# Optimization experiments

Measured on AMD Instinct MI355X. Metric: run time of the kernel, lower is better.

## Reference

```python
import jax, jax.numpy as jnp
import numpy as np

N = 100000   # nodes
E = 1600000  # edges (avg degree 16)
D = 128      # input feature dim
H = 64       # hidden dim (hard-coded in Sage.__init__)
C = 40       # output classes


def setup_inputs() -> dict:
    key = jax.random.key(0)
    ks = jax.random.split(key, 9)
    s_in = 1.0 / np.sqrt(D)
    s_h = 1.0 / np.sqrt(H)
    return {
        "x": jax.random.normal(ks[0], (N, D), jnp.float32),
        "edge_index": jax.random.randint(ks[1], (2, E), 0, N, dtype=jnp.int64),
        # SAGEConv params: lin_l acts on aggregated neighbors (carries bias),
        # lin_r acts on the root/self features (no bias), per PyG defaults.
        "W1_l": jax.random.uniform(ks[2], (D, H), jnp.float32, -s_in, s_in),
        "W1_r": jax.random.uniform(ks[3], (D, H), jnp.float32, -s_in, s_in),
        "b1": jax.random.uniform(ks[4], (H,), jnp.float32, -s_in, s_in),
        "W2_l": jax.random.uniform(ks[5], (H, C), jnp.float32, -s_h, s_h),
        "W2_r": jax.random.uniform(ks[6], (H, C), jnp.float32, -s_h, s_h),
        "b2": jax.random.uniform(ks[7], (C,), jnp.float32, -s_h, s_h),
    }


def _sage_conv(x, src, dst, W_l, W_r, b):
    # mean-aggregate neighbor features at destination nodes
    msg = x[src]                                             # [E, F] gather
    summed = jax.ops.segment_sum(msg, dst, num_segments=N)   # [N, F]
    deg = jax.ops.segment_sum(jnp.ones((src.shape[0],), x.dtype), dst,
                              num_segments=N)                # [N]
    agg = summed / jnp.maximum(deg, 1.0)[:, None]
    return agg @ W_l + x @ W_r + b


def reference(x, edge_index, W1_l, W1_r, b1, W2_l, W2_r, b2):
    src, dst = edge_index[0], edge_index[1]
    h = _sage_conv(x, src, dst, W1_l, W1_r, b1)
    h = jax.nn.relu(h)
    # F.dropout(training=False) in eval mode -> identity
    out = _sage_conv(h, src, dst, W2_l, W2_r, b2)
    return jax.nn.log_softmax(out, axis=1)
```

## Files before the change

kernel.cpp:

```cpp
#include <hip/hip_runtime.h>

__device__ __forceinline__ float bf2f(unsigned short u) {
  union { unsigned int i; float f; } c; c.i = ((unsigned int)u) << 16; return c.f;
}
__device__ __forceinline__ unsigned short f2bf(float f) {
  union { float f; unsigned int i; } c; c.f = f;
  unsigned int x = c.i;
  return (unsigned short)((x + 0x7fffu + ((x >> 16) & 1u)) >> 16);
}
__device__ __forceinline__ float lo16(unsigned int w) { return bf2f((unsigned short)(w & 0xffffu)); }
__device__ __forceinline__ float hi16(unsigned int w) { return bf2f((unsigned short)(w >> 16)); }

#define DD 128
#define HH 64
#define CC 40
#define NBUCK 512
#define NCHUNK 128
#define MAXNPB 256
#define NQ 4
#define NR 4
#define ECAP 6144

using bf16x8 = __attribute__((ext_vector_type(8))) short;
using f32x4  = __attribute__((ext_vector_type(4))) float;

__global__ __launch_bounds__(256) void detect_prepw(
    const unsigned int* e32, const unsigned int* x32, int* flags,
    const void* W1l, const void* W1r, const void* b1,
    const void* W2l, const void* W2r, const void* b2,
    unsigned short* Wb1, unsigned short* Wb2, float* b1f, float* b2f) {
  int tid = threadIdx.x;
  if (blockIdx.x == 0) {
    __shared__ unsigned int redOr[256];
    __shared__ int redCnt[256];
    unsigned int v = 0;
    for (int i = tid; i < 4096; i += 256) v |= e32[2 * i + 1];
    int cnt = 0;
    for (int i = tid; i < 4096; i += 256) {
      unsigned int w = x32[i];
      unsigned int expo = (w >> 7) & 0xffu;
      unsigned short lo = (unsigned short)(w & 0xffffu);
      if (lo == 0 || (expo >= 100u && expo <= 133u)) cnt++;
    }
    redOr[tid] = v; redCnt[tid] = cnt; __syncthreads();
    for (int s = 128; s > 0; s >>= 1) {
      if (tid < s) { redOr[tid] |= redOr[tid + s]; redCnt[tid] += redCnt[tid + s]; }
      __syncthreads();
    }
    if (tid == 0) {
      flags[0] = (redOr[0] == 0u) ? 1 : 0;
      flags[1] = (redCnt[0] < 2048) ? 1 : 0;
    }
    return;
  }
  __shared__ int red[256];
  const unsigned int* w32 = (const unsigned int*)W1l;
  int cnt = 0;
  for (int i = tid; i < 4096; i += 256) {
    unsigned int w = w32[i];
    unsigned int expo = (w >> 7) & 0xffu;
    unsigned short lo = (unsigned short)(w & 0xffffu);
    if (lo == 0 || (expo >= 100u && expo <= 133u)) cnt++;
  }
  red[tid] = cnt; __syncthreads();
  for (int s = 128; s > 0; s >>= 1) {
    if (tid < s) red[tid] += red[tid + s];
    __syncthreads();
  }
  int isf = (red[0] < 2048) ? 1 : 0;
  auto rd = [&](const void* p, int i) -> float {
    return isf ? ((const float*)p)[i] : bf2f(((const unsigned short*)p)[i]);
  };
  if (blockIdx.x == 1) {
    for (int idx = tid; idx < 128 * 128; idx += 256) {
      int n = idx >> 7, k = idx & 127;
      float v = (n < HH) ? rd(W1l, k * HH + n) : rd(W1r, k * HH + (n - HH));
      Wb1[idx] = f2bf(v);
    }
  } else {
    for (int idx = tid; idx < 48 * 128; idx += 256) {
      int n = idx >> 7, k = idx & 127;
      float v = 0.f;
      if (n < CC) v = (k < HH) ? rd(W2l, k * CC + n) : rd(W2r, (k - HH) * CC + n);
      Wb2[idx] = f2bf(v);
    }
    if (tid < HH) b1f[tid] = rd(b1, tid);
    if (tid < CC) b2f[tid] = rd(b2, tid);
  }
}

__global__ __launch_bounds__(256) void hist_or_t1(
    const int* e32, int E, int N, const int* flags, int nodesPerB, int* histG,
    const void* xraw, const unsigned short* Wb1, const float* b1f,
    unsigned short* t1, unsigned short* s1, int T1B) {
  __shared__ int cnt[NBUCK * NR];
  int b = blockIdx.x;
  int tid = threadIdx.x;

  if (b < NCHUNK) {
    for (int i = tid; i < NBUCK * NR; i += 256) cnt[i] = 0;
    __syncthreads();
    int isI64 = flags[0];
    int rep = tid & (NR - 1);
    int chunk = (E + NCHUNK - 1) / NCHUNK;
    int e0 = b * chunk, e1 = min(e0 + chunk, E);
    for (int i = e0 + tid; i < e1; i += 256) {
      int d = isI64 ? e32[2 * (E + i)] : e32[E + i];
      d = min(max(d, 0), N - 1);
      atomicAdd(&cnt[(d / nodesPerB) * NR + rep], 1);
    }
    __syncthreads();
    for (int i = tid; i < NBUCK; i += 256)
      histG[i * NCHUNK + b] =
          cnt[i * NR] + cnt[i * NR + 1] + cnt[i * NR + 2] + cnt[i * NR + 3];
    return;
  }

  int t = b - NCHUNK;
  if (t >= T1B) return;
  int lane = tid & 63, wv = tid >> 6;
  int nb = t * 64 + wv * 16;
  int oc = lane & 15, kgrp = lane >> 4;
  int node = min(nb + oc, N - 1);
  f32x4 acc[8];
#pragma unroll
  for (int i = 0; i < 8; i++) acc[i] = (f32x4){0.f, 0.f, 0.f, 0.f};

  if (flags[1]) {
    const float4* x4 = (const float4*)xraw;
#pragma unroll
    for (int kb = 0; kb < 4; kb++) {
      int k0 = kb * 32 + kgrp * 8;
      float4 a0 = x4[(size_t)node * 32 + (k0 >> 2)];
      float4 a1 = x4[(size_t)node * 32 + (k0 >> 2) + 1];
      bf16x8 af;
      af[0] = (short)f2bf(a0.x); af[1] = (short)f2bf(a0.y);
      af[2] = (short)f2bf(a0.z); af[3] = (short)f2bf(a0.w);
      af[4] = (short)f2bf(a1.x); af[5] = (short)f2bf(a1.y);
      af[6] = (short)f2bf(a1.z); af[7] = (short)f2bf(a1.w);
#pragma unroll
      for (int nblk = 0; nblk < 8; nblk++) {
        bf16x8 bfr = *(const bf16x8*)&Wb1[(nblk * 16 + oc) * 128 + k0];
        acc[nblk] = __builtin_amdgcn_mfma_f32_16x16x32_bf16(af, bfr, acc[nblk], 0, 0, 0);
      }
    }
  } else {
    const unsigned short* x16 = (const unsigned short*)xraw;
#pragma unroll
    for (int kb = 0; kb < 4; kb++) {
      int k0 = kb * 32 + kgrp * 8;
      bf16x8 af = *(const bf16x8*)&x16[(size_t)node * 128 + k0];
#pragma unroll
      for (int nblk = 0; nblk < 8; nblk++) {
        bf16x8 bfr = *(const bf16x8*)&Wb1[(nblk * 16 + oc) * 128 + k0];
        acc[nblk] = __builtin_amdgcn_mfma_f32_16x16x32_bf16(af, bfr, acc[nblk], 0, 0, 0);
      }
    }
  }

  int r0 = kgrp * 4;
#pragma unroll
  for (int nblk = 0; nblk < 8; nblk++) {
    float bias = (nblk >= 4) ? b1f[(nblk - 4) * 16 + oc] : 0.f;
#pragma unroll
    for (int r = 0; r < 4; r++) {
      int nn = nb + r0 + r;
      if (nn < N) {
        if (nblk < 4)
          t1[(size_t)nn * HH + nblk * 16 + oc] = f2bf(acc[nblk][r]);
        else
          s1[(size_t)nn * HH + (nblk - 4) * 16 + oc] = f2bf(acc[nblk][r] + bias);
      }
    }
  }
}

__global__ __launch_bounds__(128) void scanA(const int* histG, int* ohist, int* bsum) {
  __shared__ int t[NCHUNK];
  int b = blockIdx.x, tid = threadIdx.x;
  int v = histG[b * NCHUNK + tid];
  t[tid] = v; __syncthreads();
  for (int st = 1; st < NCHUNK; st <<= 1) {
    int u = (tid >= st) ? t[tid - st] : 0;
    __syncthreads();
    t[tid] += u;
    __syncthreads();
  }
  ohist[b * NCHUNK + tid] = t[tid] - v;
  if (tid == NCHUNK - 1) bsum[b] = t[tid];
}

__global__ __launch_bounds__(512) void scanB(const int* bsum, int* bbase,
                                             int* row_ptr4, int N, int E) {
  __shared__ int t[NBUCK];
  int tid = threadIdx.x;
  int v = bsum[tid];
  t[tid] = v; __syncthreads();
  for (int st = 1; st < NBUCK; st <<= 1) {
    int u = (tid >= st) ? t[tid - st] : 0;
    __syncthreads();
    t[tid] += u;
    __syncthreads();
  }
  bbase[tid] = t[tid] - v;
  if (tid == 0) { bbase[NBUCK] = E; row_ptr4[NQ * N] = E; }
}

__global__ __launch_bounds__(256) void scatter_k(const int* e32, int E, int N,
                                                 const int* flags, int nodesPerB,
                                                 int qshift,
                                                 const int* ohist, const int* bbase,
                                                 unsigned* ebuf) {
  __shared__ int cur[NBUCK];
  int tid = threadIdx.x;
  for (int i = tid; i < NBUCK; i += 256)
    cur[i] = ohist[i * NCHUNK + blockIdx.x] + bbase[i];
  __syncthreads();
  int isI64 = flags[0];
  int chunk = (E + NCHUNK - 1) / NCHUNK;
  int e0 = blockIdx.x * chunk, e1 = min(e0 + chunk, E);
  for (int i = e0 + tid; i < e1; i += 256) {
    int s, d;
    if (isI64) { s = e32[2 * i]; d = e32[2 * (E + i)]; }
    else       { s = e32[i];     d = e32[E + i]; }
    s = min(max(s, 0), N - 1);
    d = min(max(d, 0), N - 1);
    int bk = d / nodesPerB;
    int ld = d - bk * nodesPerB;
    unsigned q = (unsigned)s >> qshift;
    int p = atomicAdd(&cur[bk], 1);
    ebuf[p] = ((unsigned)ld << 19) | (q << 17) | (unsigned)s;
  }
}

__global__ __launch_bounds__(256) void bktB(
    const unsigned* ebuf, const int* bbase,
    int nodesPerB, int* row_ptr4, float* invd, int* col, int N) {
  __shared__ unsigned ecache[ECAP];
  __shared__ int cnt[MAXNPB * NQ];
  __shared__ int sA[256];
  int b = blockIdx.x;
  int tid = threadIdx.x;
  int base_node = b * nodesPerB;
  int nn = min(nodesPerB, N - base_node);
  if (nn <= 0) return;
  int nk = nn * NQ;
  int eb0 = bbase[b], eb1 = bbase[b + 1];
  int nE = eb1 - eb0;
  const unsigned* ee = ebuf + eb0;
  bool useL = (nE <= ECAP);
  for (int i = tid; i < nk; i += 256) cnt[i] = 0;
  __syncthreads();
  if (useL) {
    for (int i = tid; i < nE; i += 256) {
      unsigned v = ee[i];
      ecache[i] = v;
      atomicAdd(&cnt[v >> 17], 1);
    }
  } else {
    for (int i = tid; i < nE; i += 256) atomicAdd(&cnt[ee[i] >> 17], 1);
  }
  __syncthreads();
  for (int i = tid; i < nn; i += 256) {
    int d = cnt[NQ * i] + cnt[NQ * i + 1] + cnt[NQ * i + 2] + cnt[NQ * i + 3];
    invd[base_node + i] = 1.0f / (float)max(d, 1);
  }
  __syncthreads();
  int per = (nk + 255) / 256;
  int myb = tid * per;
  int dreg[4];
  int ssum = 0;
#pragma unroll
  for (int k = 0; k < 4; k++) {
    int idx = myb + k;
    int v = (k < per && idx < nk) ? cnt[idx] : 0;
    dreg[k] = v; ssum += v;
  }
  sA[tid] = ssum;
  __syncthreads();
  for (int st = 1; st < 256; st <<= 1) {
    int t = (tid >= st) ? sA[tid - st] : 0;
    __syncthreads();
    sA[tid] += t;
    __syncthreads();
  }
  int run = eb0 + sA[tid] - ssum;
  __syncthreads();
#pragma unroll
  for (int k = 0; k < 4; k++) {
    int idx = myb + k;
    if (k < per && idx < nk) {
      row_ptr4[(size_t)(base_node + (idx >> 2)) * NQ + (idx & 3)] = run;
      cnt[idx] = run;
      run += dreg[k];
    }
  }
  __syncthreads();
  if (useL) {
    for (int i = tid; i < nE; i += 256) {
      unsigned v = ecache[i];
      int p = atomicAdd(&cnt[v >> 17], 1);
      col[p] = (int)(v & 0x1FFFFu);
    }
  } else {
    for (int i = tid; i < nE; i += 256) {
      unsigned v = ee[i];
      int p = atomicAdd(&cnt[v >> 17], 1);
      col[p] = (int)(v & 0x1FFFFu);
    }
  }
}

__device__ __forceinline__ void gather_seg(const uint4* t8, const int* col,
                                           int s0, int s1, int r, int c,
                                           float acc[8]) {
  for (int base = s0; base < s1; base += 4) {
    int i = base + r;
    bool g = (i < s1);
    int nb = g ? col[i] : 0;
    uint4 v = make_uint4(0, 0, 0, 0);
    if (g) v = t8[(size_t)nb * 8 + c];
    acc[0] += lo16(v.x); acc[1] += hi16(v.x);
    acc[2] += lo16(v.y); acc[3] += hi16(v.y);
    acc[4] += lo16(v.z); acc[5] += hi16(v.z);
    acc[6] += lo16(v.w); acc[7] += hi16(v.w);
  }
}

__global__ __launch_bounds__(256) void aggregate1(const unsigned short* t1,
                                                  const unsigned short* s1,
                                                  const int* row_ptr4, const float* invd,
                                                  const int* col, unsigned short* h, int N) {
  int wave = threadIdx.x >> 6, lane = threadIdx.x & 63;
  int ns = lane >> 5, r = (lane >> 3) & 3, c = lane & 7;
  int n = blockIdx.x * 8 + wave * 2 + ns;
  if (n >= N) return;
  int4 rp = *(const int4*)&row_ptr4[(size_t)NQ * n];
  int e4 = row_ptr4[(size_t)NQ * n + 4];
  float acc[8] = {0, 0, 0, 0, 0, 0, 0, 0};
  const uint4* t8 = (const uint4*)t1;
  gather_seg(t8, col, rp.x, rp.y, r, c, acc);
  gather_seg(t8, col, rp.y, rp.z, r, c, acc);
  gather_seg(t8, col, rp.z, rp.w, r, c, acc);
  gather_seg(t8, col, rp.w, e4, r, c, acc);
#pragma unroll
  for (int m = 8; m <= 16; m <<= 1)
#pragma unroll
    for (int i = 0; i < 8; i++) acc[i] += __shfl_xor(acc[i], m, 64);

  if (r == 0) {
    float id = invd[n];
    uint4 sv = ((const uint4*)s1)[(size_t)n * 8 + c];
    float s[8] = {lo16(sv.x), hi16(sv.x), lo16(sv.y), hi16(sv.y),
                  lo16(sv.z), hi16(sv.z), lo16(sv.w), hi16(sv.w)};
    unsigned int o[4];
#pragma unroll
    for (int i = 0; i < 4; i++) {
      float a0 = fmaxf(acc[2 * i] * id + s[2 * i], 0.f);
      float a1 = fmaxf(acc[2 * i + 1] * id + s[2 * i + 1], 0.f);
      o[i] = (unsigned int)f2bf(a0) | ((unsigned int)f2bf(a1) << 16);
    }
    ((uint4*)h)[(size_t)n * 8 + c] = make_uint4(o[0], o[1], o[2], o[3]);
  }
}

__global__ __launch_bounds__(256) void agg2f(const unsigned short* h,
                                             const int* row_ptr4, const float* invd,
                                             const int* col,
                                             const unsigned short* Wb2,
                                             const float* b2f,
                                             float* out, int N) {
  __shared__ unsigned lds[64 * 33];
  int tid = threadIdx.x, wv = tid >> 6, lane = tid & 63;
  int ns = lane >> 5, r = (lane >> 3) & 3, c = lane & 7;
  int nb = blockIdx.x * 64;
  const uint4* h8 = (const uint4*)h;

  for (int rr = 0; rr < 8; rr++) {
    int ln = wv * 16 + rr * 2 + ns;
    int n = nb + ln;
    float acc[8] = {0, 0, 0, 0, 0, 0, 0, 0};
    int4 rp; int e4;
    if (n < N) {
      rp = *(const int4*)&row_ptr4[(size_t)NQ * n];
      e4 = row_ptr4[(size_t)NQ * n + 4];
    } else {
      rp = make_int4(0, 0, 0, 0); e4 = 0;
    }
    gather_seg(h8, col, rp.x, rp.y, r, c, acc);
    gather_seg(h8, col, rp.y, rp.z, r, c, acc);
    gather_seg(h8, col, rp.z, rp.w, r, c, acc);
    gather_seg(h8, col, rp.w, e4, r, c, acc);
#pragma unroll
    for (int m = 8; m <= 16; m <<= 1)
#pragma unroll
      for (int i = 0; i < 8; i++) acc[i] += __shfl_xor(acc[i], m, 64);
    if (r == 0) {
      float id = (n < N) ? invd[n] : 0.f;
#pragma unroll
      for (int q = 0; q < 4; q++) {
        unsigned u = (unsigned)f2bf(acc[2 * q] * id) |
                     ((unsigned)f2bf(acc[2 * q + 1] * id) << 16);
        lds[ln * 33 + c * 4 + q] = u;
      }
    }
  }
  __syncthreads();

  int oc = lane & 15, kgrp = lane >> 4;
  int noderow = wv * 16 + oc;
  int node = min(nb + noderow, N - 1);
  f32x4 acc3[3];
#pragma unroll
  for (int i = 0; i < 3; i++) acc3[i] = (f32x4){0.f, 0.f, 0.f, 0.f};

#pragma unroll
  for (int kb = 0; kb < 4; kb++) {
    int k0 = kb * 32 + kgrp * 8;
    bf16x8 af;
    if (kb < 2) {
      union { unsigned u[4]; bf16x8 v; } cv;
      int base = noderow * 33 + (k0 >> 1);
      cv.u[0] = lds[base]; cv.u[1] = lds[base + 1];
      cv.u[2] = lds[base + 2]; cv.u[3] = lds[base + 3];
      af = cv.v;
    } else {
      af = *(const bf16x8*)&h[(size_t)node * HH + (k0 - 64)];
    }
#pragma unroll
    for (int nblk = 0; nblk < 3; nblk++) {
      bf16x8 bfr = *(const bf16x8*)&Wb2[(nblk * 16 + oc) * 128 + k0];
      acc3[nblk] = __builtin_amdgcn_mfma_f32_16x16x32_bf16(af, bfr, acc3[nblk], 0, 0, 0);
    }
  }

#pragma unroll
  for (int nblk = 0; nblk < 3; nblk++) {
    int cc = nblk * 16 + oc;
    float bias = (cc < CC) ? b2f[cc] : 0.f;
#pragma unroll
    for (int rg = 0; rg < 4; rg++) acc3[nblk][rg] += bias;
  }

#pragma unroll
  for (int rg = 0; rg < 4; rg++) {
    int nn = nb + wv * 16 + kgrp * 4 + rg;
    float m = -INFINITY;
#pragma unroll
    for (int nblk = 0; nblk < 3; nblk++)
      if (nblk * 16 + oc < CC) m = fmaxf(m, acc3[nblk][rg]);
    for (int off = 1; off <= 8; off <<= 1) m = fmaxf(m, __shfl_xor(m, off, 64));
    float s = 0.f;
#pragma unroll
    for (int nblk = 0; nblk < 3; nblk++)
      if (nblk * 16 + oc < CC) s += __expf(acc3[nblk][rg] - m);
    for (int off = 1; off <= 8; off <<= 1) s += __shfl_xor(s, off, 64);
    float lse = m + __logf(s);
    if (nn < N) {
#pragma unroll
      for (int nblk = 0; nblk < 3; nblk++) {
        int cc = nblk * 16 + oc;
        if (cc < CC) out[(size_t)nn * CC + cc] = acc3[nblk][rg] - lse;
      }
    }
  }
}

extern "C" void kernel_launch(void* const* d_in, const int* in_sizes, int n_in,
                              void* d_out, int out_size, void* d_ws, size_t ws_size,
                              hipStream_t stream) {
  const void* x   = d_in[0];
  const int*  e   = (const int*)d_in[1];
  const void* W1l = d_in[2];
  const void* W1r = d_in[3];
  const void* b1  = d_in[4];
  const void* W2l = d_in[5];
  const void* W2r = d_in[6];
  const void* b2  = d_in[7];
  float* out = (float*)d_out;

  const int N = in_sizes[0] / DD;
  const int E = in_sizes[1] / 2;
  const int nodesPerB = (N + NBUCK - 1) / NBUCK;
  const int nbuck = (N + nodesPerB - 1) / nodesPerB;
  const int T1B = (N + 63) / 64;
  int qshift = 0;
  while (((unsigned)(N - 1) >> qshift) > 3u) qshift++;

  char* w = (char*)d_ws;
  size_t off = 0;
  auto carve = [&](size_t bytes) -> void* {
    void* p = (void*)(w + off);
    off += (bytes + 255) & ~(size_t)255;
    return p;
  };
  int* col      = (int*)carve((size_t)E * 4);
  int* row_ptr4 = (int*)carve(((size_t)N * NQ + 1) * 4);
  float* invd   = (float*)carve((size_t)N * 4);
  int* histG    = (int*)carve((size_t)NBUCK * NCHUNK * 4);
  int* ohist    = (int*)carve((size_t)NBUCK * NCHUNK * 4);
  int* bsum     = (int*)carve(NBUCK * 4);
  int* bbase    = (int*)carve((NBUCK + 1) * 4);
  int* flags    = (int*)carve(8);
  unsigned short* t1   = (unsigned short*)carve((size_t)N * HH * 2);
  unsigned short* s1   = (unsigned short*)carve((size_t)N * HH * 2);
  unsigned short* h    = (unsigned short*)carve((size_t)N * HH * 2);
  unsigned short* Wb1  = (unsigned short*)carve(128 * 128 * 2);
  unsigned short* Wb2  = (unsigned short*)carve(48 * 128 * 2);
  float* b1f   = (float*)carve(HH * sizeof(float));
  float* b2f   = (float*)carve(CC * sizeof(float));
  unsigned* ebuf = (unsigned*)carve((size_t)E * 4);
  (void)ws_size; (void)n_in; (void)out_size;

  detect_prepw<<<3, 256, 0, stream>>>((const unsigned int*)e, (const unsigned int*)x,
                                      flags, W1l, W1r, b1, W2l, W2r, b2,
                                      Wb1, Wb2, b1f, b2f);
  hist_or_t1<<<NCHUNK + T1B, 256, 0, stream>>>(e, E, N, flags, nodesPerB, histG,
                                               x, Wb1, b1f, t1, s1, T1B);
  scanA<<<NBUCK, 128, 0, stream>>>(histG, ohist, bsum);
  scanB<<<1, 512, 0, stream>>>(bsum, bbase, row_ptr4, N, E);
  scatter_k<<<NCHUNK, 256, 0, stream>>>(e, E, N, flags, nodesPerB, qshift,
                                        ohist, bbase, ebuf);
  bktB<<<nbuck, 256, 0, stream>>>(ebuf, bbase, nodesPerB, row_ptr4, invd, col, N);
  aggregate1<<<(N + 7) / 8, 256, 0, stream>>>(t1, s1, row_ptr4, invd, col, h, N);
  agg2f<<<(N + 63) / 64, 256, 0, stream>>>(h, row_ptr4, invd, col, Wb2, b2f, out, N);
}
```

Baseline: 311.3 us.

## Fuse histogram into prep kernel and overlap scatter with layer-1 GEMM

The destination histogram moves into the weight-prep/detect launch, with each histogram block recomputing the int64 flag locally. The edge scatter is fused into the same launch as the layer-1 feature transform (t1/s1), so the scatter overlaps with the GEMM work and one launch is removed. The chunk count doubles to 256 to spread histogram and scatter over more blocks. Bucket division is replaced by a precomputed reciprocal multiply-high. The cost is more histogram columns to scan and a redundant flag reduction in every histogram block.

Result: faster. 293.6 us (-5.7%).

```diff
diff --git a/kernel.cpp b/kernel.cpp
--- a/kernel.cpp
+++ b/kernel.cpp
@@ -15,7 +15,7 @@
 #define HH 64
 #define CC 40
 #define NBUCK 512
-#define NCHUNK 128
+#define NCHUNK 256
 #define MAXNPB 256
 #define NQ 4
 #define NR 4
@@ -24,95 +24,161 @@
 using bf16x8 = __attribute__((ext_vector_type(8))) short;
 using f32x4  = __attribute__((ext_vector_type(4))) float;
 
-__global__ __launch_bounds__(256) void detect_prepw(
-    const unsigned int* e32, const unsigned int* x32, int* flags,
+__global__ __launch_bounds__(256) void detect_prepw_hist(
+    const unsigned int* e32u, const unsigned int* x32, int* flags,
     const void* W1l, const void* W1r, const void* b1,
     const void* W2l, const void* W2r, const void* b2,
-    unsigned short* Wb1, unsigned short* Wb2, float* b1f, float* b2f) {
+    unsigned short* Wb1, unsigned short* Wb2, float* b1f, float* b2f,
+    const int* e32, int E, int N, unsigned mulM, int* histG) {
+  __shared__ int cnt[NBUCK * NR];
   int tid = threadIdx.x;
-  if (blockIdx.x == 0) {
-    __shared__ unsigned int redOr[256];
-    __shared__ int redCnt[256];
+  int b = blockIdx.x;
+
+  if (b == 0) {
     unsigned int v = 0;
-    for (int i = tid; i < 4096; i += 256) v |= e32[2 * i + 1];
-    int cnt = 0;
+    for (int i = tid; i < 4096; i += 256) v |= e32u[2 * i + 1];
+    int c2 = 0;
     for (int i = tid; i < 4096; i += 256) {
       unsigned int w = x32[i];
       unsigned int expo = (w >> 7) & 0xffu;
       unsigned short lo = (unsigned short)(w & 0xffffu);
-      if (lo == 0 || (expo >= 100u && expo <= 133u)) cnt++;
-    }
-    redOr[tid] = v; redCnt[tid] = cnt; __syncthreads();
+      if (lo == 0 || (expo >= 100u && expo <= 133u)) c2++;
+    }
+    cnt[tid] = (int)v; cnt[256 + tid] = c2; __syncthreads();
     for (int s = 128; s > 0; s >>= 1) {
-      if (tid < s) { redOr[tid] |= redOr[tid + s]; redCnt[tid] += redCnt[tid + s]; }
+      if (tid < s) { cnt[tid] |= cnt[tid + s]; cnt[256 + tid] += cnt[256 + tid + s]; }
       __syncthreads();
     }
     if (tid == 0) {
-      flags[0] = (redOr[0] == 0u) ? 1 : 0;
-      flags[1] = (redCnt[0] < 2048) ? 1 : 0;
+      flags[0] = (cnt[0] == 0) ? 1 : 0;
+      flags[1] = (cnt[256] < 2048) ? 1 : 0;
     }
     return;
   }
-  __shared__ int red[256];
-  const unsigned int* w32 = (const unsigned int*)W1l;
-  int cnt = 0;
-  for (int i = tid; i < 4096; i += 256) {
-    unsigned int w = w32[i];
-    unsigned int expo = (w >> 7) & 0xffu;
-    unsigned short lo = (unsigned short)(w & 0xffffu);
-    if (lo == 0 || (expo >= 100u && expo <= 133u)) cnt++;
-  }
-  red[tid] = cnt; __syncthreads();
+
+  if (b <= 2) {
+    const unsigned int* w32 = (const unsigned int*)W1l;
+    int c2 = 0;
+    for (int i = tid; i < 4096; i += 256) {
+      unsigned int w = w32[i];
+      unsigned int expo = (w >> 7) & 0xffu;
+      unsigned short lo = (unsigned short)(w & 0xffffu);
+      if (lo == 0 || (expo >= 100u && expo <= 133u)) c2++;
+    }
+    cnt[tid] = c2; __syncthreads();
+    for (int s = 128; s > 0; s >>= 1) {
+      if (tid < s) cnt[tid] += cnt[tid + s];
+      __syncthreads();
+    }
+    int isf = (cnt[0] < 2048) ? 1 : 0;
+    auto rd = [&](const void* p, int i) -> float {
+      return isf ? ((const float*)p)[i] : bf2f(((const unsigned short*)p)[i]);
+    };
+    if (b == 1) {
+      for (int idx = tid; idx < 128 * 128; idx += 256) {
+        int n = idx >> 7, k = idx & 127;
+        float v = (n < HH) ? rd(W1l, k * HH + n) : rd(W1r, k * HH + (n - HH));
+        Wb1[idx] = f2bf(v);
+      }
+    } else {
+      for (int idx = tid; idx < 48 * 128; idx += 256) {
+        int n = idx >> 7, k = idx & 127;
+        float v = 0.f;
+        if (n < CC) v = (k < HH) ? rd(W2l, k * CC + n) : rd(W2r, (k - HH) * CC + n);
+        Wb2[idx] = f2bf(v);
+      }
+      if (tid < HH) b1f[tid] = rd(b1, tid);
+      if (tid < CC) b2f[tid] = rd(b2, tid);
+    }
+    return;
+  }
+
+  int hb = b - 3;
+  unsigned int v = 0;
+  for (int i = tid; i < 4096; i += 256) v |= e32u[2 * i + 1];
+  cnt[tid] = (int)v; __syncthreads();
   for (int s = 128; s > 0; s >>= 1) {
-    if (tid < s) red[tid] += red[tid + s];
-    __syncthreads();
-  }
-  int isf = (red[0] < 2048) ? 1 : 0;
-  auto rd = [&](const void* p, int i) -> float {
-    return isf ? ((const float*)p)[i] : bf2f(((const unsigned short*)p)[i]);
-  };
-  if (blockIdx.x == 1) {
-    for (int idx = tid; idx < 128 * 128; idx += 256) {
-      int n = idx >> 7, k = idx & 127;
-      float v = (n < HH) ? rd(W1l, k * HH + n) : rd(W1r, k * HH + (n - HH));
-      Wb1[idx] = f2bf(v);
-    }
-  } else {
-    for (int idx = tid; idx < 48 * 128; idx += 256) {
-      int n = idx >> 7, k = idx & 127;
-      float v = 0.f;
-      if (n < CC) v = (k < HH) ? rd(W2l, k * CC + n) : rd(W2r, (k - HH) * CC + n);
-      Wb2[idx] = f2bf(v);
-    }
-    if (tid < HH) b1f[tid] = rd(b1, tid);
-    if (tid < CC) b2f[tid] = rd(b2, tid);
-  }
-}
-
-__global__ __launch_bounds__(256) void hist_or_t1(
-    const int* e32, int E, int N, const int* flags, int nodesPerB, int* histG,
+    if (tid < s) cnt[tid] |= cnt[tid + s];
+    __syncthreads();
+  }
+  int isI64 = (cnt[0] == 0) ? 1 : 0;
+  __syncthreads();
+  for (int i = tid; i < NBUCK * NR; i += 256) cnt[i] = 0;
+  __syncthreads();
+  int rep = tid & (NR - 1);
+  int chunk = (E + NCHUNK - 1) / NCHUNK;
+  int e0 = hb * chunk, e1 = min(e0 + chunk, E);
+  for (int i = e0 + tid; i < e1; i += 256) {
+    int d = isI64 ? e32[2 * (E + i)] : e32[E + i];
+    d = min(max(d, 0), N - 1);
+    int bk = (int)__umulhi((unsigned)d, mulM);
+    atomicAdd(&cnt[bk * NR + rep], 1);
+  }
+  __syncthreads();
+  for (int i = tid; i < NBUCK; i += 256)
+    histG[i * NCHUNK + hb] =
+        cnt[i * NR] + cnt[i * NR + 1] + cnt[i * NR + 2] + cnt[i * NR + 3];
+}
+
+__global__ __launch_bounds__(256) void scanA(const int* histG, int* ohist, int* bsum) {
+  __shared__ int t[NCHUNK];
+  int b = blockIdx.x, tid = threadIdx.x;
+  int v = histG[b * NCHUNK + tid];
+  t[tid] = v; __syncthreads();
+  for (int st = 1; st < NCHUNK; st <<= 1) {
+    int u = (tid >= st) ? t[tid - st] : 0;
+    __syncthreads();
+    t[tid] += u;
+    __syncthreads();
+  }
+  ohist[b * NCHUNK + tid] = t[tid] - v;
+  if (tid == NCHUNK - 1) bsum[b] = t[tid];
+}
+
+__global__ __launch_bounds__(512) void scanB(const int* bsum, int* bbase,
+                                             int* row_ptr4, int N, int E) {
+  __shared__ int t[NBUCK];
+  int tid = threadIdx.x;
+  int v = bsum[tid];
+  t[tid] = v; __syncthreads();
+  for (int st = 1; st < NBUCK; st <<= 1) {
+    int u = (tid >= st) ? t[tid - st] : 0;
+    __syncthreads();
+    t[tid] += u;
+    __syncthreads();
+  }
+  bbase[tid] = t[tid] - v;
+  if (tid == 0) { bbase[NBUCK] = E; row_ptr4[NQ * N] = E; }
+}
+
+__global__ __launch_bounds__(256) void scat_or_t1(
+    const int* e32, int E, int N, const int* flags, int nodesPerB,
+    unsigned mulM, int qshift, const int* ohist, const int* bbase, unsigned* ebuf,
     const void* xraw, const unsigned short* Wb1, const float* b1f,
     unsigned short* t1, unsigned short* s1, int T1B) {
-  __shared__ int cnt[NBUCK * NR];
+  __shared__ int cur[NBUCK];
   int b = blockIdx.x;
   int tid = threadIdx.x;
 
   if (b < NCHUNK) {
-    for (int i = tid; i < NBUCK * NR; i += 256) cnt[i] = 0;
+    for (int i = tid; i < NBUCK; i += 256)
+      cur[i] = ohist[i * NCHUNK + b] + bbase[i];
     __syncthreads();
     int isI64 = flags[0];
-    int rep = tid & (NR - 1);
     int chunk = (E + NCHUNK - 1) / NCHUNK;
     int e0 = b * chunk, e1 = min(e0 + chunk, E);
     for (int i = e0 + tid; i < e1; i += 256) {
-      int d = isI64 ? e32[2 * (E + i)] : e32[E + i];
+      int s, d;
+      if (isI64) { s = e32[2 * i]; d = e32[2 * (E + i)]; }
+      else       { s = e32[i];     d = e32[E + i]; }
+      s = min(max(s, 0), N - 1);
       d = min(max(d, 0), N - 1);
-      atomicAdd(&cnt[(d / nodesPerB) * NR + rep], 1);
-    }
-    __syncthreads();
-    for (int i = tid; i < NBUCK; i += 256)
-      histG[i * NCHUNK + b] =
-          cnt[i * NR] + cnt[i * NR + 1] + cnt[i * NR + 2] + cnt[i * NR + 3];
+      int bk = (int)__umulhi((unsigned)d, mulM);
+      int ld = d - bk * nodesPerB;
+      unsigned q = (unsigned)s >> qshift;
+      int p = atomicAdd(&cur[bk], 1);
+      ebuf[p] = ((unsigned)ld << 19) | (q << 17) | (unsigned)s;
+    }
     return;
   }
 
@@ -172,64 +238,6 @@
           s1[(size_t)nn * HH + (nblk - 4) * 16 + oc] = f2bf(acc[nblk][r] + bias);
       }
     }
-  }
-}
-
-__global__ __launch_bounds__(128) void scanA(const int* histG, int* ohist, int* bsum) {
-  __shared__ int t[NCHUNK];
-  int b = blockIdx.x, tid = threadIdx.x;
-  int v = histG[b * NCHUNK + tid];
-  t[tid] = v; __syncthreads();
-  for (int st = 1; st < NCHUNK; st <<= 1) {
-    int u = (tid >= st) ? t[tid - st] : 0;
-    __syncthreads();
-    t[tid] += u;
-    __syncthreads();
-  }
-  ohist[b * NCHUNK + tid] = t[tid] - v;
-  if (tid == NCHUNK - 1) bsum[b] = t[tid];
-}
-
-__global__ __launch_bounds__(512) void scanB(const int* bsum, int* bbase,
-                                             int* row_ptr4, int N, int E) {
-  __shared__ int t[NBUCK];
-  int tid = threadIdx.x;
-  int v = bsum[tid];
-  t[tid] = v; __syncthreads();
-  for (int st = 1; st < NBUCK; st <<= 1) {
-    int u = (tid >= st) ? t[tid - st] : 0;
-    __syncthreads();
-    t[tid] += u;
-    __syncthreads();
-  }
-  bbase[tid] = t[tid] - v;
-  if (tid == 0) { bbase[NBUCK] = E; row_ptr4[NQ * N] = E; }
-}
-
-__global__ __launch_bounds__(256) void scatter_k(const int* e32, int E, int N,
-                                                 const int* flags, int nodesPerB,
-                                                 int qshift,
-                                                 const int* ohist, const int* bbase,
-                                                 unsigned* ebuf) {
-  __shared__ int cur[NBUCK];
-  int tid = threadIdx.x;
-  for (int i = tid; i < NBUCK; i += 256)
-    cur[i] = ohist[i * NCHUNK + blockIdx.x] + bbase[i];
-  __syncthreads();
-  int isI64 = flags[0];
-  int chunk = (E + NCHUNK - 1) / NCHUNK;
-  int e0 = blockIdx.x * chunk, e1 = min(e0 + chunk, E);
-  for (int i = e0 + tid; i < e1; i += 256) {
-    int s, d;
-    if (isI64) { s = e32[2 * i]; d = e32[2 * (E + i)]; }
-    else       { s = e32[i];     d = e32[E + i]; }
-    s = min(max(s, 0), N - 1);
-    d = min(max(d, 0), N - 1);
-    int bk = d / nodesPerB;
-    int ld = d - bk * nodesPerB;
-    unsigned q = (unsigned)s >> qshift;
-    int p = atomicAdd(&cur[bk], 1);
-    ebuf[p] = ((unsigned)ld << 19) | (q << 17) | (unsigned)s;
   }
 }
 
@@ -483,6 +491,8 @@
   const int E = in_sizes[1] / 2;
   const int nodesPerB = (N + NBUCK - 1) / NBUCK;
   const int nbuck = (N + nodesPerB - 1) / nodesPerB;
+  const unsigned mulM =
+      (unsigned)(((1ULL << 32) + (unsigned)nodesPerB - 1) / (unsigned)nodesPerB);
   const int T1B = (N + 63) / 64;
   int qshift = 0;
   while (((unsigned)(N - 1) >> qshift) > 3u) qshift++;
@@ -512,15 +522,15 @@
   unsigned* ebuf = (unsigned*)carve((size_t)E * 4);
   (void)ws_size; (void)n_in; (void)out_size;
 
-  detect_prepw<<<3, 256, 0, stream>>>((const unsigned int*)e, (const unsigned int*)x,
-                                      flags, W1l, W1r, b1, W2l, W2r, b2,
-                                      Wb1, Wb2, b1f, b2f);
-  hist_or_t1<<<NCHUNK + T1B, 256, 0, stream>>>(e, E, N, flags, nodesPerB, histG,
+  detect_prepw_hist<<<3 + NCHUNK, 256, 0, stream>>>(
+      (const unsigned int*)e, (const unsigned int*)x, flags,
+      W1l, W1r, b1, W2l, W2r, b2, Wb1, Wb2, b1f, b2f,
+      e, E, N, mulM, histG);
+  scanA<<<NBUCK, NCHUNK, 0, stream>>>(histG, ohist, bsum);
+  scanB<<<1, 512, 0, stream>>>(bsum, bbase, row_ptr4, N, E);
+  scat_or_t1<<<NCHUNK + T1B, 256, 0, stream>>>(e, E, N, flags, nodesPerB,
+                                               mulM, qshift, ohist, bbase, ebuf,
                                                x, Wb1, b1f, t1, s1, T1B);
-  scanA<<<NBUCK, 128, 0, stream>>>(histG, ohist, bsum);
-  scanB<<<1, 512, 0, stream>>>(bsum, bbase, row_ptr4, N, E);
-  scatter_k<<<NCHUNK, 256, 0, stream>>>(e, E, N, flags, nodesPerB, qshift,
-                                        ohist, bbase, ebuf);
   bktB<<<nbuck, 256, 0, stream>>>(ebuf, bbase, nodesPerB, row_ptr4, invd, col, N);
   aggregate1<<<(N + 7) / 8, 256, 0, stream>>>(t1, s1, row_ptr4, invd, col, h, N);
   agg2f<<<(N + 63) / 64, 256, 0, stream>>>(h, row_ptr4, invd, col, Wb2, b2f, out, N);
```
